# Performance work log

Measured on AMD Instinct MI355X. Metric: run time of the kernel, lower is better.

The kernel has to match this reference:

```python
import jax, jax.numpy as jnp
import numpy as np

N = 4096; E = 32768; H = 128; R = 32; L = 2
CUT_UP = 5.0; MAX_Z = 100

def cosine_cutoff(d):
    c = 0.5 * (jnp.cos(d * (np.pi / CUT_UP)) + 1.0)
    return c * (d < CUT_UP).astype(d.dtype)

def tensor_norm(t):
    return (t * t).sum((-2, -1))

def decompose_tensor(t):
    eye = jnp.eye(3, dtype=t.dtype)
    I = (jnp.trace(t, axis1=-2, axis2=-1) / 3.0)[..., None, None] * eye
    tT = jnp.swapaxes(t, -2, -1)
    A = 0.5 * (t - tT)
    S = 0.5 * (t + tT) - I
    return I, A, S

def vector_to_skewtensor(v):
    x, y, z = v[..., 0], v[..., 1], v[..., 2]
    o = jnp.zeros_like(x)
    return jnp.stack([o, -z, y, z, o, -x, -y, x, o], axis=-1).reshape(v.shape[:-1] + (3, 3))

def vector_to_symtensor(v):
    t = v[..., :, None] * v[..., None, :]
    eye = jnp.eye(3, dtype=v.dtype)
    I = (jnp.trace(t, axis1=-2, axis2=-1) / 3.0)[..., None, None] * eye
    return t - I  # symmetric already, 0.5*(t+t^T) == t

def cmix(T, W):  # nn.Linear(H,H,bias=False) over the channel dim of [N,H,3,3]
    return jnp.einsum('nhij,hk->nkij', T, W)

def layernorm(x, g, b, eps=1e-5):
    m = x.mean(-1, keepdims=True)
    v = ((x - m) ** 2).mean(-1, keepdims=True)
    return (x - m) / jnp.sqrt(v + eps) * g + b

def setup_inputs():
    key = jax.random.key(0)
    ks = iter(jax.random.split(key, 48))
    def nrm(shape, fan_in):
        return jax.random.normal(next(ks), shape, jnp.float32) / np.sqrt(fan_in)
    inp = {}
    inp['z'] = jax.random.randint(next(ks), (N,), 0, MAX_Z)
    inp['edge_index'] = jax.random.randint(next(ks), (2, E), 0, N)
    inp['edge_weight'] = jax.random.uniform(next(ks), (E,), jnp.float32) * CUT_UP
    inp['edge_vec'] = jax.random.normal(next(ks), (E, 3), jnp.float32)
    inp['edge_attr'] = jax.random.normal(next(ks), (E, R), jnp.float32)
    inp['emb_table'] = nrm((MAX_Z, H), H)
    inp['dp1_w'] = nrm((R, H), R); inp['dp1_b'] = jnp.zeros((H,))
    inp['dp2_w'] = nrm((R, H), R); inp['dp2_b'] = jnp.zeros((H,))
    inp['dp3_w'] = nrm((R, H), R); inp['dp3_b'] = jnp.zeros((H,))
    inp['emb2_w'] = nrm((2 * H, H), 2 * H); inp['emb2_b'] = jnp.zeros((H,))
    inp['tne_lt'] = nrm((3, H, H), H)
    inp['tne_s0_w'] = nrm((H, 2 * H), H); inp['tne_s0_b'] = jnp.zeros((2 * H,))
    inp['tne_s1_w'] = nrm((2 * H, 3 * H), 2 * H); inp['tne_s1_b'] = jnp.zeros((3 * H,))
    inp['ln_g'] = jnp.ones((H,)); inp['ln_b'] = jnp.zeros((H,))
    inp['msg_l0_w'] = nrm((L, R, H), R); inp['msg_l0_b'] = jnp.zeros((L, H))
    inp['msg_l1_w'] = nrm((L, H, 2 * H), H); inp['msg_l1_b'] = jnp.zeros((L, 2 * H))
    inp['msg_l2_w'] = nrm((L, 2 * H, 3 * H), 2 * H); inp['msg_l2_b'] = jnp.zeros((L, 3 * H))
    inp['msg_lx'] = nrm((L, 3, H, H), H)
    inp['msg_lt'] = nrm((L, 3, H, H), H)
    return inp

def _forward(z, edge_index, edge_weight, edge_vec, edge_attr, emb_table,
             dp1_w, dp1_b, dp2_w, dp2_b, dp3_w, dp3_b, emb2_w, emb2_b,
             tne_lt, tne_s0_w, tne_s0_b, tne_s1_w, tne_s1_b, ln_g, ln_b,
             msg_l0_w, msg_l0_b, msg_l1_w, msg_l1_b, msg_l2_w, msg_l2_b,
             msg_lx, msg_lt):
    src, dst = edge_index[0], edge_index[1]
    eye = jnp.eye(3, dtype=jnp.float32)
    segsum = lambda x: jax.ops.segment_sum(x, dst, num_segments=N)
    silu = jax.nn.silu
    # ---- TensorNeighborEmbedding ----
    Z = emb_table[z]                                     # [N,H]
    C = cosine_cutoff(edge_weight)                       # [E]
    W1 = (edge_attr @ dp1_w + dp1_b) * C[:, None]
    W2 = (edge_attr @ dp2_w + dp2_b) * C[:, None]
    W3 = (edge_attr @ dp3_w + dp3_b) * C[:, None]
    mask = (src != dst)[:, None]
    vn = jnp.linalg.norm(edge_vec, axis=-1, keepdims=True)
    ev = jnp.where(mask, edge_vec / jnp.maximum(vn, 1e-12), edge_vec)
    skew = vector_to_skewtensor(ev)                      # [E,3,3]
    sym = vector_to_symtensor(ev)                        # [E,3,3]
    Zij = jnp.concatenate([Z[dst], Z[src]], axis=-1) @ emb2_w + emb2_b  # [E,H]
    # I channel is a scaled identity per edge -> factor the eye out of the scatter
    In = segsum(Zij * W1)[..., None, None] * eye                         # [N,H,3,3]
    An = segsum((Zij * W2)[:, :, None, None] * skew[:, None])            # [N,H,3,3]
    Sn = segsum((Zij * W3)[:, :, None, None] * sym[:, None])             # [N,H,3,3]
    norm = layernorm(tensor_norm(In + An + Sn), ln_g, ln_b)              # [N,H]
    In = cmix(In, tne_lt[0]); An = cmix(An, tne_lt[1]); Sn = cmix(Sn, tne_lt[2])
    fsc = silu(silu(norm @ tne_s0_w + tne_s0_b) @ tne_s1_w + tne_s1_b).reshape(N, H, 3)
    X = (fsc[..., 0, None, None] * In + fsc[..., 1, None, None] * An
         + fsc[..., 2, None, None] * Sn)
    # ---- TensorMessage layers ----
    for l in range(L):
        ea = silu(edge_attr @ msg_l0_w[l] + msg_l0_b[l])
        ea = silu(ea @ msg_l1_w[l] + msg_l1_b[l])
        ea = silu(ea @ msg_l2_w[l] + msg_l2_b[l])
        ea = (ea * C[:, None]).reshape(E, H, 3)
        X = X / (tensor_norm(X) + 1.0)[..., None, None]
        I, A, S = decompose_tensor(X)
        I = cmix(I, msg_lx[l, 0]); A = cmix(A, msg_lx[l, 1]); S = cmix(S, msg_lx[l, 2])
        Y = I + A + S
        Im = segsum(ea[:, :, 0, None, None] * I[src])    # gather -> scale -> scatter
        Am = segsum(ea[:, :, 1, None, None] * A[src])
        Sm = segsum(ea[:, :, 2, None, None] * S[src])
        msg = Im + Am + Sm
        AB = msg @ Y + Y @ msg                           # batched 3x3 matmuls
        I, A, S = decompose_tensor(AB)
        d = (tensor_norm(I + A + S) + 1.0)[..., None, None]
        I = cmix(I / d, msg_lt[l, 0]); A = cmix(A / d, msg_lt[l, 1]); S = cmix(S / d, msg_lt[l, 2])
        dX = I + A + S
        dX = dX + dX @ dX
        X = X + dX
    return X

def reference(z, edge_index, edge_weight, edge_vec, edge_attr, emb_table,
              dp1_w, dp1_b, dp2_w, dp2_b, dp3_w, dp3_b, emb2_w, emb2_b,
              tne_lt, tne_s0_w, tne_s0_b, tne_s1_w, tne_s1_b, ln_g, ln_b,
              msg_l0_w, msg_l0_b, msg_l1_w, msg_l1_b, msg_l2_w, msg_l2_b,
              msg_lx, msg_lt):
    return _forward(z, edge_index, edge_weight, edge_vec, edge_attr, emb_table,
                    dp1_w, dp1_b, dp2_w, dp2_b, dp3_w, dp3_b, emb2_w, emb2_b,
                    tne_lt, tne_s0_w, tne_s0_b, tne_s1_w, tne_s1_b, ln_g, ln_b,
                    msg_l0_w, msg_l0_b, msg_l1_w, msg_l1_b, msg_l2_w, msg_l2_b,
                    msg_lx, msg_lt)
```

## Files before the change

kernel.cpp:

```cpp
#include <hip/hip_runtime.h>
#include <hip/hip_bf16.h>

typedef __hip_bfloat16 bf16;
typedef __attribute__((ext_vector_type(8))) short short8v;
typedef __attribute__((ext_vector_type(4))) float f32x4;

#define NN 4096
#define NE 32768
#define HH 128
#define MAXZ 100
#define TPB 8
#define NB 1


__device__ __forceinline__ float b2f(bf16 v){ return __bfloat162float(v); }
__device__ __forceinline__ float ldf(const float* p, size_t i){ return p[i]; }
__device__ __forceinline__ float ldf(const bf16*  p, size_t i){ return __bfloat162float(p[i]); }
__device__ __forceinline__ float siluf(float x){ return x * __builtin_amdgcn_rcpf(1.0f + __expf(-x)); }
__device__ __forceinline__ unsigned short f2bu(float x){
  bf16 h = __float2bfloat16(x);
  return *reinterpret_cast<unsigned short*>(&h);
}
__device__ __forceinline__ float bround(float x){
  bf16 h = __float2bfloat16(x);
// ... 17 lines not shown
__global__ void __launch_bounds__(256) k_count(const int* __restrict__ dst, int* __restrict__ counts){
  int e = blockIdx.x*256 + threadIdx.x;
  if (e < NE) atomicAdd(&counts[dst[e]], 1);
}

__global__ void __launch_bounds__(1024) k_scan(const int* __restrict__ counts, int* __restrict__ offsets, int* __restrict__ cursor){
  __shared__ int lds[1024];
  int t = threadIdx.x;
  int c0 = counts[4*t+0], c1 = counts[4*t+1], c2 = counts[4*t+2], c3 = counts[4*t+3];
  int s1 = c0+c1, s2 = s1+c2, s3 = s2+c3;
  lds[t] = s3;
  __syncthreads();
  for (int off=1; off<1024; off<<=1){
    int v = lds[t];
    int add = (t>=off)? lds[t-off] : 0;
    __syncthreads();
    lds[t] = v + add;
    __syncthreads();
  }
  int incl = lds[t];
  int base = incl - s3;
  offsets[4*t+0]=base;    offsets[4*t+1]=base+c0; offsets[4*t+2]=base+s1; offsets[4*t+3]=base+s2;
  cursor [4*t+0]=base;    cursor [4*t+1]=base+c0; cursor [4*t+2]=base+s1; cursor [4*t+3]=base+s2;
  if (t==1023) offsets[4096]=incl;
}

__global__ void __launch_bounds__(256) k_fill(const int* __restrict__ dst, const int* __restrict__ src,
                                              int* __restrict__ cursor,
                                              int* __restrict__ pos, int* __restrict__ csrc){
  int e = blockIdx.x*256 + threadIdx.x;
  if (e < NE){
    int p = atomicAdd(&cursor[dst[e]], 1);
    pos[e] = p;
    csrc[p] = src[e];
  }
}

template<typename T>
__device__ __forceinline__ void geom_impl(const T* ew, const T* evec,
    const int* src, const int* dst, const int* pos, float* gC, float* gVp){
  int e = blockIdx.x*256 + threadIdx.x;
  if (e >= NE) return;
  float d = ldf(ew, e);
  float c = 0.5f*(cosf(d*0.6283185307179586f)+1.0f);
  c = (d < 5.0f) ? c : 0.0f;
  gC[e] = c;
  float x = ldf(evec, (size_t)e*3+0), y = ldf(evec, (size_t)e*3+1), z = ldf(evec, (size_t)e*3+2);
  if (src[e] != dst[e]){
    float n = sqrtf(x*x+y*y+z*z);
    float inv = 1.0f/fmaxf(n, 1e-12f);
    x*=inv; y*=inv; z*=inv;
  }
  int p = pos[e];
  gVp[p*3+0]=x; gVp[p*3+1]=y; gVp[p*3+2]=z;
}
__global__ void __launch_bounds__(256) k_geom(const void* ew, const void* evec,
    const int* __restrict__ src, const int* __restrict__ dst, const int* __restrict__ pos,
    float* __restrict__ gC, float* __restrict__ gVp, const int* __restrict__ flag){
  if (flag[0]) geom_impl<float>((const float*)ew, (const float*)evec, src, dst, pos, gC, gVp);
  else         geom_impl<bf16 >((const bf16* )ew, (const bf16* )evec, src, dst, pos, gC, gVp);
}

template<typename T>
__device__ __forceinline__ void zemb_impl(const T* emb, const T* emb2_w,
    float* P1z, float* P2z, float* Zr){
  int zv = blockIdx.x, h = threadIdx.x;
  Zr[h] = ldf(emb, (size_t)zv*HH + h);
  __syncthreads();
  float p1=0.f, p2=0.f;
  for (int r=0;r<128;++r){
    float x = Zr[r];
    p1 += x*ldf(emb2_w, (size_t)r*HH+h);
    p2 += x*ldf(emb2_w, (size_t)(r+128)*HH+h);
  }
  P1z[zv*HH+h]=p1; P2z[zv*HH+h]=p2;
}
__global__ void __launch_bounds__(128) k_zemb(const void* emb, const void* emb2_w,
    float* __restrict__ P1z, float* __restrict__ P2z, const int* __restrict__ flag){
  __shared__ float Zr[128];
  if (flag[0]) zemb_impl<float>((const float*)emb, (const float*)emb2_w, P1z, P2z, Zr);
  else         zemb_impl<bf16 >((const bf16* )emb, (const bf16* )emb2_w, P1z, P2z, Zr);
}

__global__ void __launch_bounds__(256) k_cvt_attr(const void* in, unsigned short* __restrict__ out,
                                                  const int* __restrict__ flag){
  int i = blockIdx.x*256 + threadIdx.x;
  if (flag[0]) out[i] = f2bu(((const float*)in)[i]);
  else         out[i] = ((const unsigned short*)in)[i];
}

struct PackDescs {
  const void*     base[23];
  long            eoff[23];
  unsigned short* out[23];
  int K[23]; int N[23];
};
template<typename T>
__device__ __forceinline__ void pack_impl(const PackDescs& d){
  int y = blockIdx.y;
  int K = d.K[y], N = d.N[y];
  int ktiles = K>>5, ntiles = N>>4;
  int total = ktiles*ntiles*64;
  int idx = blockIdx.x*256 + threadIdx.x;
  if (idx >= total) return;
  int lane = idx & 63, tile = idx >> 6;
  int kt = tile % ktiles, nt = tile / ktiles;
  const T* W = (const T*)d.base[y] + d.eoff[y];
  int n = nt*16 + (lane&15), k0 = kt*32 + (lane>>4)*8;
  unsigned int t[8];
  #pragma unroll
  for (int j=0;j<8;++j) t[j] = f2bu(ldf(W, (size_t)(k0+j)*N + n));
  uint4 v;
  v.x = t[0] | (t[1]<<16);
  v.y = t[2] | (t[3]<<16);
  v.z = t[4] | (t[5]<<16);
  v.w = t[6] | (t[7]<<16);
  *reinterpret_cast<uint4*>(d.out[y] + ((size_t)tile*64 + lane)*8) = v;
}
__global__ void __launch_bounds__(256) k_pack(PackDescs d, const int* __restrict__ flag){
  if (flag[0]) pack_impl<float>(d);
  else         pack_impl<bf16 >(d);
}

template<typename T>
__device__ __forceinline__ void tne_edge_impl(
  const T* eattr, const int* src, const int* dst, const int* z, const int* pos,
  const T* dp1_w, const T* dp1_b, const T* dp2_w, const T* dp2_b,
  const T* dp3_w, const T* dp3_b, const T* emb2_b,
  const float* P1z, const float* P2z, const float* gC, bf16* eabuf,
  float (*attr)[32], int* zd, int* zs, int* ppos)
{
  int e0 = blockIdx.x*TPB;
  int h  = threadIdx.x;
  for (int i=h; i<TPB*32; i+=128) attr[i>>5][i&31] = ldf(eattr, (size_t)e0*32 + i);
  if (h < TPB){ int e=e0+h; zd[h]=z[dst[e]]; zs[h]=z[src[e]]; ppos[h]=pos[e]; }
  __syncthreads();
  float w1[TPB], w2[TPB], w3[TPB];
  float b1v=ldf(dp1_b,h), b2v=ldf(dp2_b,h), b3v=ldf(dp3_b,h);
  #pragma unroll
  for (int e=0;e<TPB;++e){ w1[e]=b1v; w2[e]=b2v; w3[e]=b3v; }
  for (int r=0;r<32;++r){
    float u1=ldf(dp1_w,(size_t)r*HH+h), u2=ldf(dp2_w,(size_t)r*HH+h), u3=ldf(dp3_w,(size_t)r*HH+h);
    #pragma unroll
    for (int e=0;e<TPB;++e){ float a=attr[e][r]; w1[e]+=a*u1; w2[e]+=a*u2; w3[e]+=a*u3; }
  }
  float eb = ldf(emb2_b,h);
  #pragma unroll
  for (int e=0;e<TPB;++e){
    float zij = P1z[zd[e]*HH+h] + P2z[zs[e]*HH+h] + eb;
    float c = gC[e0+e];
    bf16* p = eabuf + (size_t)ppos[e]*384;
    p[h]     = __float2bfloat16(zij*w1[e]*c);
    p[128+h] = __float2bfloat16(zij*w2[e]*c);
    p[256+h] = __float2bfloat16(zij*w3[e]*c);
  }
}
__global__ void __launch_bounds__(128) k_tne_edge(
  const void* eattr, const int* __restrict__ src, const int* __restrict__ dst,
  const int* __restrict__ z, const int* __restrict__ pos,
  const void* dp1_w, const void* dp1_b, const void* dp2_w, const void* dp2_b,
  const void* dp3_w, const void* dp3_b, const void* emb2_b,
  const float* __restrict__ P1z, const float* __restrict__ P2z,
  const float* __restrict__ gC, bf16* __restrict__ eabuf, const int* __restrict__ flag)
{
  __shared__ float attr[TPB][32];
  __shared__ int zd[TPB], zs[TPB], ppos[TPB];
  if (flag[0]) tne_edge_impl<float>((const float*)eattr, src, dst, z, pos,
      (const float*)dp1_w, (const float*)dp1_b, (const float*)dp2_w, (const float*)dp2_b,
      (const float*)dp3_w, (const float*)dp3_b, (const float*)emb2_b, P1z, P2z, gC, eabuf, attr, zd, zs, ppos);
  else tne_edge_impl<bf16>((const bf16*)eattr, src, dst, z, pos,
      (const bf16*)dp1_w, (const bf16*)dp1_b, (const bf16*)dp2_w, (const bf16*)dp2_b,
      (const bf16*)dp3_w, (const bf16*)dp3_b, (const bf16*)emb2_b, P1z, P2z, gC, eabuf, attr, zd, zs, ppos);
}

template<typename T>
__device__ __forceinline__ void tne_scat_impl(
  const int* offsets, const float* gVp, const bf16* eabuf,
  const T* ln_g, const T* ln_b, bf16* sm10, bf16* lnO, float* red)
{
  int n0 = blockIdx.x*NB, h = threadIdx.x;
  float tnv[NB];
  #pragma unroll
  for (int nn=0;nn<NB;++nn){
    int n = n0+nn;
    float a=0, v0=0,v1=0,v2=0, s0=0,s1=0,s2=0,s3=0,s4=0,s5=0;
    int beg = offsets[n], end = offsets[n+1];
    int i = beg;
    for (; i+4 <= end; i += 4){
      float c1[4],c2[4],c3[4],vx[4],vy[4],vz[4];
      #pragma unroll
      for (int u=0;u<4;++u){
        const bf16* p = eabuf + (size_t)(i+u)*384;
        c1[u]=b2f(p[h]); c2[u]=b2f(p[128+h]); c3[u]=b2f(p[256+h]);
        vx[u]=gVp[(i+u)*3+0]; vy[u]=gVp[(i+u)*3+1]; vz[u]=gVp[(i+u)*3+2];
      }
      #pragma unroll
      for (int u=0;u<4;++u){
        float tr3 = (vx[u]*vx[u]+vy[u]*vy[u]+vz[u]*vz[u])*(1.0f/3.0f);
        a  += c1[u];
        v0 += c2[u]*vx[u]; v1 += c2[u]*vy[u]; v2 += c2[u]*vz[u];
        s0 += c3[u]*(vx[u]*vx[u] - tr3); s1 += c3[u]*vx[u]*vy[u]; s2 += c3[u]*vx[u]*vz[u];
        s3 += c3[u]*(vy[u]*vy[u] - tr3); s4 += c3[u]*vy[u]*vz[u]; s5 += c3[u]*(vz[u]*vz[u] - tr3);
      }
    }
    for (; i<end; ++i){
      const bf16* p = eabuf + (size_t)i*384;
      float c1 = b2f(p[h]), c2 = b2f(p[128+h]), c3 = b2f(p[256+h]);
      float vx = gVp[i*3+0], vy = gVp[i*3+1], vz = gVp[i*3+2];
      float tr3 = (vx*vx+vy*vy+vz*vz)*(1.0f/3.0f);
      a  += c1;
      v0 += c2*vx; v1 += c2*vy; v2 += c2*vz;
      s0 += c3*(vx*vx - tr3); s1 += c3*vx*vy;          s2 += c3*vx*vz;
      s3 += c3*(vy*vy - tr3); s4 += c3*vy*vz;          s5 += c3*(vz*vz - tr3);
    }
    bf16* sp = sm10 + (size_t)n*1280;
    sp[0*128+h]=__float2bfloat16(a);
    sp[1*128+h]=__float2bfloat16(v0); sp[2*128+h]=__float2bfloat16(v1); sp[3*128+h]=__float2bfloat16(v2);
    sp[4*128+h]=__float2bfloat16(s0); sp[5*128+h]=__float2bfloat16(s1); sp[6*128+h]=__float2bfloat16(s2);
    sp[7*128+h]=__float2bfloat16(s3); sp[8*128+h]=__float2bfloat16(s4); sp[9*128+h]=__float2bfloat16(s5);
    tnv[nn] = 3.0f*a*a + 2.0f*(v0*v0+v1*v1+v2*v2)
            + s0*s0 + s3*s3 + s5*s5 + 2.0f*(s1*s1 + s2*s2 + s4*s4);
  }
  float gg = ldf(ln_g,h), bb = ldf(ln_b,h);
  #pragma unroll
  for (int nn=0;nn<NB;++nn){
    __syncthreads();
    red[h] = tnv[nn]; __syncthreads();
    for (int off=64; off>=1; off>>=1){ if (h<off) red[h]+=red[h+off]; __syncthreads(); }
    float mean = red[0]*(1.0f/128.0f);
    __syncthreads();
    float dm = tnv[nn] - mean;
    red[h] = dm*dm; __syncthreads();
    for (int off=64; off>=1; off>>=1){ if (h<off) red[h]+=red[h+off]; __syncthreads(); }
    float var = red[0]*(1.0f/128.0f);
    lnO[(size_t)(n0+nn)*128 + h] = __float2bfloat16(dm*rsqrtf(var+1e-5f)*gg + bb);
  }
}
__global__ void __launch_bounds__(128) k_tne_scat(
  const int* __restrict__ offsets, const float* __restrict__ gVp, const bf16* __restrict__ eabuf,
  const void* ln_g, const void* ln_b, bf16* __restrict__ sm10, bf16* __restrict__ lnO,
  const int* __restrict__ flag)
{
  __shared__ float red[128];
  if (flag[0]) tne_scat_impl<float>(offsets, gVp, eabuf, (const float*)ln_g, (const float*)ln_b, sm10, lnO, red);
  else         tne_scat_impl<bf16 >(offsets, gVp, eabuf, (const bf16* )ln_g, (const bf16* )ln_b, sm10, lnO, red);
}

template<typename T>
__device__ __forceinline__ void node_mlp_impl(
  const bf16* lnO, const unsigned short* ps0, const unsigned short* ps1,
  const T* b0, const T* b1, bf16* fsc3, unsigned short* h2p)
{
  int wid  = threadIdx.x >> 6;
  int lane = threadIdx.x & 63;
  int n0 = blockIdx.x*16;
  int m = lane & 15, g = lane >> 4;
  short8v aln[4];
  #pragma unroll
  for (int ks=0; ks<4; ++ks)
    aln[ks] = *reinterpret_cast<const short8v*>((const unsigned short*)lnO + (size_t)(n0+m)*128 + ks*32 + g*8);
  for (int nt=wid; nt<16; nt+=4){
    float bias = ldf(b0, nt*16+m);
    f32x4 acc = {bias,bias,bias,bias};
    #pragma unroll
    for (int ks=0; ks<4; ++ks){
      short8v b = *reinterpret_cast<const short8v*>(ps0 + ((size_t)(nt*4+ks)*64 + lane)*8);
      acc = __builtin_amdgcn_mfma_f32_16x16x32_bf16(aln[ks], b, acc, 0,0,0);
    }
    #pragma unroll
    for (int r=0;r<4;++r){
      int n = nt*16 + m, row = g*4 + r;
      h2p[(n>>5)*512 + (((n>>3)&3)*16+row)*8 + (n&7)] = f2bu(siluf(acc[r]));
    }
  }
  __syncthreads();
  short8v a3[8];
  #pragma unroll
  for (int ks=0; ks<8; ++ks) a3[ks] = *reinterpret_cast<const short8v*>(&h2p[ks*512 + lane*8]);
  for (int nt=wid; nt<24; nt+=4){
    float bias = ldf(b1, nt*16+m);
    f32x4 acc = {bias,bias,bias,bias};
    #pragma unroll
    for (int ks=0; ks<8; ++ks){
      short8v b = *reinterpret_cast<const short8v*>(ps1 + ((size_t)(nt*8+ks)*64 + lane)*8);
      acc = __builtin_amdgcn_mfma_f32_16x16x32_bf16(a3[ks], b, acc, 0,0,0);
    }
    #pragma unroll
    for (int r=0;r<4;++r){
      int n = nt*16 + m, row = g*4 + r;
      ((unsigned short*)fsc3)[(size_t)(n0+row)*384 + (n%3)*128 + (n/3)] = f2bu(siluf(acc[r]));
    }
  }
}
__global__ void __launch_bounds__(256) k_node_mlp(
  const bf16* __restrict__ lnO, const unsigned short* __restrict__ ps0,
  const unsigned short* __restrict__ ps1,
  const void* b0, const void* b1, bf16* __restrict__ fsc3, const int* __restrict__ flag)
{
  __shared__ __align__(16) unsigned short h2p[4096];
  if (flag[0]) node_mlp_impl<float>(lnO, ps0, ps1, (const float*)b0, (const float*)b1, fsc3, h2p);
  else         node_mlp_impl<bf16 >(lnO, ps0, ps1, (const bf16* )b0, (const bf16* )b1, fsc3, h2p);
}

__global__ void __launch_bounds__(256) k_tne_cmix(
  const bf16* __restrict__ sm10, const unsigned short* __restrict__ pwlt,
  const bf16* __restrict__ fsc3, float* __restrict__ X9)
{
  int wid  = threadIdx.x >> 6;
  int lane = threadIdx.x & 63;
  int n0 = blockIdx.x*16;
  int m = lane & 15, g = lane >> 4;
  f32x4 acc[10][2];
  #pragma unroll
  for (int c=0;c<10;++c){ acc[c][0]=(f32x4){0,0,0,0}; acc[c][1]=(f32x4){0,0,0,0}; }
  #pragma unroll
  for (int c=0;c<10;++c){
    int mat = (c==0) ? 0 : (c<4) ? 1 : 2;
    const unsigned short* bw = pwlt + (size_t)mat*16384;
    short8v af[4];
    #pragma unroll
    for (int ks=0; ks<4; ++ks)
      af[ks] = *reinterpret_cast<const short8v*>((const unsigned short*)sm10 + (size_t)(n0+m)*1280 + c*128 + ks*32 + g*8);
    #pragma unroll
    for (int t=0;t<2;++t){
      int nt = wid + t*4;
      #pragma unroll
      for (int ks=0; ks<4; ++ks){
        short8v b = *reinterpret_cast<const short8v*>(bw + ((size_t)(nt*4+ks)*64 + lane)*8);
        acc[c][t] = __builtin_amdgcn_mfma_f32_16x16x32_bf16(af[ks], b, acc[c][t], 0,0,0);
      }
    }
  }
  #pragma unroll
  for (int t=0;t<2;++t){
    int nt = wid + t*4;
    int h = nt*16 + m;
    #pragma unroll
    for (int r=0;r<4;++r){
      int node = n0 + g*4 + r;
      float am  = acc[0][t][r];
      float wm0 = acc[1][t][r], wm1 = acc[2][t][r], wm2 = acc[3][t][r];
      float t0 = acc[4][t][r], t1 = acc[5][t][r], t2 = acc[6][t][r];
      float t3 = acc[7][t][r], t4 = acc[8][t][r], t5 = acc[9][t][r];
      float f0 = b2f(fsc3[(size_t)node*384 + h]);
      float f1 = b2f(fsc3[(size_t)node*384 + 128 + h]);
      float f2 = b2f(fsc3[(size_t)node*384 + 256 + h]);
      float* xp = X9 + (size_t)node*1152;
      xp[0*128+h] = f0*am + f2*t0;
      xp[1*128+h] = -f1*wm2 + f2*t1;
      xp[2*128+h] =  f1*wm1 + f2*t2;
      xp[3*128+h] =  f1*wm2 + f2*t1;
      xp[4*128+h] = f0*am + f2*t3;
      xp[5*128+h] = -f1*wm0 + f2*t4;
      xp[6*128+h] = -f1*wm1 + f2*t2;
      xp[7*128+h] =  f1*wm0 + f2*t4;
      xp[8*128+h] = f0*am + f2*t5;
    }
  }
}

__global__ void __launch_bounds__(256) k_cmix_norm(
  float* __restrict__ X9, const unsigned short* __restrict__ pw, bf16* __restrict__ Y10)
{
  __shared__ __align__(16) unsigned short sst[16*1280];
  int n0 = blockIdx.x*16;
  int tid = threadIdx.x;
  #pragma unroll
  for (int it=0; it<8; ++it){
    int idx = it*256 + tid;
    int nn = idx >> 7, h = idx & 127;
    float* xp = X9 + (size_t)(n0+nn)*1152;
    float x00=xp[0*128+h], x01=xp[1*128+h], x02=xp[2*128+h];
    float x10=xp[3*128+h], x11=xp[4*128+h], x12=xp[5*128+h];
    float x20=xp[6*128+h], x21=xp[7*128+h], x22=xp[8*128+h];
    float tn = x00*x00+x01*x01+x02*x02+x10*x10+x11*x11+x12*x12+x20*x20+x21*x21+x22*x22;
    float inv = __builtin_amdgcn_rcpf(tn+1.0f);
    x00*=inv; x01*=inv; x02*=inv; x10*=inv; x11*=inv; x12*=inv; x20*=inv; x21*=inv; x22*=inv;
    xp[0*128+h]=x00; xp[1*128+h]=x01; xp[2*128+h]=x02;
    xp[3*128+h]=x10; xp[4*128+h]=x11; xp[5*128+h]=x12;
    xp[6*128+h]=x20; xp[7*128+h]=x21; xp[8*128+h]=x22;
    float a = (x00+x11+x22)*(1.0f/3.0f);
    unsigned short* sp = sst + (size_t)nn*1280;
    sp[0*128+h]=f2bu(a);
    sp[1*128+h]=f2bu(0.5f*(x21-x12));
    sp[2*128+h]=f2bu(0.5f*(x02-x20));
    sp[3*128+h]=f2bu(0.5f*(x10-x01));
    sp[4*128+h]=f2bu(x00-a);
    sp[5*128+h]=f2bu(0.5f*(x01+x10));
    sp[6*128+h]=f2bu(0.5f*(x02+x20));
    sp[7*128+h]=f2bu(x11-a);
    sp[8*128+h]=f2bu(0.5f*(x12+x21));
    sp[9*128+h]=f2bu(x22-a);
  }
  __syncthreads();
  int wid  = tid >> 6;
  int lane = tid & 63;
  int m = lane & 15, g = lane >> 4;
  f32x4 acc[10][2];
  #pragma unroll
  for (int c=0;c<10;++c){ acc[c][0]=(f32x4){0,0,0,0}; acc[c][1]=(f32x4){0,0,0,0}; }
  #pragma unroll
  for (int c=0;c<10;++c){
    int mat = (c==0) ? 0 : (c<4) ? 1 : 2;
    const unsigned short* bw = pw + (size_t)mat*16384;
    short8v af[4];
    #pragma unroll
    for (int ks=0; ks<4; ++ks)
      af[ks] = *reinterpret_cast<const short8v*>(&sst[(size_t)m*1280 + c*128 + ks*32 + g*8]);
    #pragma unroll
    for (int t=0;t<2;++t){
      int nt = wid + t*4;
      #pragma unroll
      for (int ks=0; ks<4; ++ks){
        short8v b = *reinterpret_cast<const short8v*>(bw + ((size_t)(nt*4+ks)*64 + lane)*8);
        acc[c][t] = __builtin_amdgcn_mfma_f32_16x16x32_bf16(af[ks], b, acc[c][t], 0,0,0);
      }
    }
  }
  #pragma unroll
  for (int t=0;t<2;++t){
    int nt = wid + t*4;
    int h = nt*16 + m;
    #pragma unroll
    for (int r=0;r<4;++r){
      int node = n0 + g*4 + r;
      unsigned short* op = (unsigned short*)Y10 + (size_t)node*1280;
      #pragma unroll
      for (int c=0;c<10;++c) op[c*128 + h] = f2bu(acc[c][t][r]);
    }
  }
}

template<typename T>
__device__ __forceinline__ void mfma_impl(
  const unsigned short* eattr_c, const float* gC, const int* pos,
  const unsigned short* p0, const unsigned short* p1, const unsigned short* p2,
  const T* b0, const T* b1, const T* b2,
  unsigned short* eabuf, unsigned short* buf, int* spos)
{
  int wid  = threadIdx.x >> 6;
  int lane = threadIdx.x & 63;
  int e0 = blockIdx.x*16;
  int m = lane & 15, g = lane >> 4;
  if (threadIdx.x < 16) spos[threadIdx.x] = pos[e0 + threadIdx.x];
  float cc[4];
  #pragma unroll
  for (int r=0;r<4;++r) cc[r] = gC[e0 + g*4 + r];
  unsigned short* h1p = buf;
  unsigned short* h2p = buf + 2048;
  short8v a1 = *reinterpret_cast<const short8v*>(eattr_c + (size_t)(e0+m)*32 + g*8);
  for (int nt=wid; nt<8; nt+=4){
    float bias = ldf(b0, nt*16+m);
    f32x4 acc = {bias,bias,bias,bias};
    short8v b = *reinterpret_cast<const short8v*>(p0 + ((size_t)nt*64 + lane)*8);
    acc = __builtin_amdgcn_mfma_f32_16x16x32_bf16(a1, b, acc, 0,0,0);
    #pragma unroll
    for (int r=0;r<4;++r){
      int n = nt*16 + m, row = g*4 + r;
      h1p[(n>>5)*512 + (((n>>3)&3)*16+row)*8 + (n&7)] = f2bu(siluf(acc[r]));
    }
  }
  __syncthreads();
  short8v a2[4];
  #pragma unroll
  for (int ks=0; ks<4; ++ks) a2[ks] = *reinterpret_cast<const short8v*>(&h1p[ks*512 + lane*8]);
  for (int nt=wid; nt<16; nt+=4){
    float bias = ldf(b1, nt*16+m);
    f32x4 acc = {bias,bias,bias,bias};
    #pragma unroll
    for (int ks=0; ks<4; ++ks){
      short8v b = *reinterpret_cast<const short8v*>(p1 + ((size_t)(nt*4+ks)*64 + lane)*8);
      acc = __builtin_amdgcn_mfma_f32_16x16x32_bf16(a2[ks], b, acc, 0,0,0);
    }
    #pragma unroll
    for (int r=0;r<4;++r){
      int n = nt*16 + m, row = g*4 + r;
      h2p[(n>>5)*512 + (((n>>3)&3)*16+row)*8 + (n&7)] = f2bu(siluf(acc[r]));
    }
  }
  __syncthreads();
  short8v a3[8];
  #pragma unroll
  for (int ks=0; ks<8; ++ks) a3[ks] = *reinterpret_cast<const short8v*>(&h2p[ks*512 + lane*8]);
  __syncthreads();
  for (int nt=wid; nt<24; nt+=4){
    float bias = ldf(b2, nt*16+m);
    f32x4 acc = {bias,bias,bias,bias};
    #pragma unroll
    for (int ks=0; ks<8; ++ks){
      short8v b = *reinterpret_cast<const short8v*>(p2 + ((size_t)(nt*8+ks)*64 + lane)*8);
      acc = __builtin_amdgcn_mfma_f32_16x16x32_bf16(a3[ks], b, acc, 0,0,0);
    }
    #pragma unroll
    for (int r=0;r<4;++r){
      int n = nt*16 + m, row = g*4 + r;
      float v = siluf(acc[r]) * cc[r];
      buf[row*408 + (n%3)*136 + (n/3)] = f2bu(v);
    }
  }
  __syncthreads();
  int r  = threadIdx.x >> 4;
  int ch = threadIdx.x & 15;
  size_t base = (size_t)spos[r]*384;
  #pragma unroll
  for (int seg=0; seg<3; ++seg){
    uint4 v = *reinterpret_cast<const uint4*>(&buf[r*408 + seg*136 + ch*8]);
    *reinterpret_cast<uint4*>(eabuf + base + (size_t)(seg*128 + ch*8)) = v;
  }
}
__global__ void __launch_bounds__(256) k_msg_edge_mfma(
  const unsigned short* __restrict__ eattr_c, const float* __restrict__ gC,
  const int* __restrict__ pos,
  const unsigned short* __restrict__ p0a, const unsigned short* __restrict__ p0b,
  const unsigned short* __restrict__ p1a, const unsigned short* __restrict__ p1b,
  const unsigned short* __restrict__ p2a, const unsigned short* __restrict__ p2b,
  const void* b0, const void* b1, const void* b2,
  unsigned short* __restrict__ eabuf_msg, const int* __restrict__ flag)
{
  __shared__ __align__(16) unsigned short buf[6528];
  __shared__ int spos[16];
  int l = blockIdx.y;
  const unsigned short* p0 = l ? p0b : p0a;
  const unsigned short* p1 = l ? p1b : p1a;
  const unsigned short* p2 = l ? p2b : p2a;
  unsigned short* eabuf = eabuf_msg + (size_t)l*NE*384;
  if (flag[0]) mfma_impl<float>(eattr_c, gC, pos, p0, p1, p2,
      (const float*)b0 + (long)l*128, (const float*)b1 + (long)l*256, (const float*)b2 + (long)l*384,
      eabuf, buf, spos);
  else mfma_impl<bf16>(eattr_c, gC, pos, p0, p1, p2,
      (const bf16*)b0 + (long)l*128, (const bf16*)b1 + (long)l*256, (const bf16*)b2 + (long)l*384,
      eabuf, buf, spos);
}

__global__ void __launch_bounds__(128) k_msg_sab(
  const int* __restrict__ offsets, const int* __restrict__ csrc,
  const bf16* __restrict__ eabuf, const bf16* __restrict__ Y10, bf16* __restrict__ smb)
{
  int n0 = blockIdx.x*NB, h = threadIdx.x;
  #pragma unroll
  for (int nn=0;nn<NB;++nn){
    int n = n0+nn;
    float am=0, vm0=0,vm1=0,vm2=0, smm0=0,smm1=0,smm2=0,smm3=0,smm4=0,smm5=0;
    int beg = offsets[n], end = offsets[n+1];
    int i = beg;
    for (; i+4 <= end; i += 4){
      int ss[4];
      #pragma unroll
      for (int u=0;u<4;++u){ ss[u] = csrc[i+u]; }
      float e0a[4], e1a[4], e2a[4];
      float y0[4],y1[4],y2[4],y3[4],y4[4],y5[4],y6[4],y7[4],y8[4],y9[4];
      #pragma unroll
      for (int u=0;u<4;++u){
        const bf16* ep = eabuf + (size_t)(i+u)*384;
        e0a[u]=b2f(ep[h]); e1a[u]=b2f(ep[128+h]); e2a[u]=b2f(ep[256+h]);
        const bf16* yp = Y10 + (size_t)ss[u]*1280;
        y0[u]=b2f(yp[0*128+h]); y1[u]=b2f(yp[1*128+h]); y2[u]=b2f(yp[2*128+h]);
        y3[u]=b2f(yp[3*128+h]); y4[u]=b2f(yp[4*128+h]); y5[u]=b2f(yp[5*128+h]);
        y6[u]=b2f(yp[6*128+h]); y7[u]=b2f(yp[7*128+h]); y8[u]=b2f(yp[8*128+h]);
        y9[u]=b2f(yp[9*128+h]);
      }
      #pragma unroll
      for (int u=0;u<4;++u){
        am   += e0a[u]*y0[u];
        vm0  += e1a[u]*y1[u]; vm1 += e1a[u]*y2[u]; vm2 += e1a[u]*y3[u];
        smm0 += e2a[u]*y4[u]; smm1 += e2a[u]*y5[u]; smm2 += e2a[u]*y6[u];
        smm3 += e2a[u]*y7[u]; smm4 += e2a[u]*y8[u]; smm5 += e2a[u]*y9[u];
      }
    }
    for (; i<end; ++i){
      int s = csrc[i];
      const bf16* ep = eabuf + (size_t)i*384;
      float e0 = b2f(ep[h]), e1 = b2f(ep[128+h]), e2 = b2f(ep[256+h]);
      const bf16* yp = Y10 + (size_t)s*1280;
      am   += e0*b2f(yp[0*128+h]);
      vm0  += e1*b2f(yp[1*128+h]); vm1 += e1*b2f(yp[2*128+h]); vm2 += e1*b2f(yp[3*128+h]);
      smm0 += e2*b2f(yp[4*128+h]); smm1 += e2*b2f(yp[5*128+h]); smm2 += e2*b2f(yp[6*128+h]);
      smm3 += e2*b2f(yp[7*128+h]); smm4 += e2*b2f(yp[8*128+h]); smm5 += e2*b2f(yp[9*128+h]);
    }
    const bf16* yp = Y10 + (size_t)n*1280;
    float aY=b2f(yp[0*128+h]), u0=b2f(yp[1*128+h]), u1=b2f(yp[2*128+h]), u2=b2f(yp[3*128+h]);
    float q0=b2f(yp[4*128+h]), q1=b2f(yp[5*128+h]), q2=b2f(yp[6*128+h]);
    float q3=b2f(yp[7*128+h]), q4=b2f(yp[8*128+h]), q5=b2f(yp[9*128+h]);
    float m00=am+smm0,   m01=-vm2+smm1, m02= vm1+smm2;
    float m10= vm2+smm1, m11=am+smm3,  m12=-vm0+smm4;
    float m20=-vm1+smm2, m21= vm0+smm4, m22=am+smm5;
    float y00=aY+q0,  y01=-u2+q1, y02= u1+q2;
    float y10= u2+q1, y11=aY+q3,  y12=-u0+q4;
    float y20=-u1+q2, y21= u0+q4, y22=aY+q5;
    float ab00 = m00*y00+m01*y10+m02*y20 + y00*m00+y01*m10+y02*m20;
    float ab01 = m00*y01+m01*y11+m02*y21 + y00*m01+y01*m11+y02*m21;
    float ab02 = m00*y02+m01*y12+m02*y22 + y00*m02+y01*m12+y02*m22;
    float ab10 = m10*y00+m11*y10+m12*y20 + y10*m00+y11*m10+y12*m20;
    float ab11 = m10*y01+m11*y11+m12*y21 + y10*m01+y11*m11+y12*m21;
    float ab12 = m10*y02+m11*y12+m12*y22 + y10*m02+y11*m12+y12*m22;
    float ab20 = m20*y00+m21*y10+m22*y20 + y20*m00+y21*m10+y22*m20;
    float ab21 = m20*y01+m21*y11+m22*y21 + y20*m01+y21*m11+y22*m21;
    float ab22 = m20*y02+m21*y12+m22*y22 + y20*m02+y21*m12+y22*m22;
    float a2 = (ab00+ab11+ab22)*(1.0f/3.0f);
    float w0 = 0.5f*(ab21-ab12), w1 = 0.5f*(ab02-ab20), w2 = 0.5f*(ab10-ab01);
    float t0 = ab00-a2, t1 = 0.5f*(ab01+ab10), t2 = 0.5f*(ab02+ab20);
    float t3 = ab11-a2, t4 = 0.5f*(ab12+ab21), t5 = ab22-a2;
    float dnm = ab00*ab00+ab01*ab01+ab02*ab02+ab10*ab10+ab11*ab11+ab12*ab12
              + ab20*ab20+ab21*ab21+ab22*ab22 + 1.0f;
    float inv = __builtin_amdgcn_rcpf(dnm);
    bf16* sp = smb + (size_t)n*1280;
    sp[0*128+h]=__float2bfloat16(a2*inv);
    sp[1*128+h]=__float2bfloat16(w0*inv); sp[2*128+h]=__float2bfloat16(w1*inv); sp[3*128+h]=__float2bfloat16(w2*inv);
    sp[4*128+h]=__float2bfloat16(t0*inv); sp[5*128+h]=__float2bfloat16(t1*inv); sp[6*128+h]=__float2bfloat16(t2*inv);
    sp[7*128+h]=__float2bfloat16(t3*inv); sp[8*128+h]=__float2bfloat16(t4*inv); sp[9*128+h]=__float2bfloat16(t5*inv);
  }
}

template<typename T>
__device__ __forceinline__ void cmix_fin_impl(
  const bf16* smb, const unsigned short* pw, float* X9, T* out, int write_out)
{
  int wid  = threadIdx.x >> 6;
  int lane = threadIdx.x & 63;
  int n0 = blockIdx.x*16;
  int m = lane & 15, g = lane >> 4;
  f32x4 acc[10][2];
  #pragma unroll
  for (int c=0;c<10;++c){ acc[c][0]=(f32x4){0,0,0,0}; acc[c][1]=(f32x4){0,0,0,0}; }
  #pragma unroll
  for (int c=0;c<10;++c){
    int mat = (c==0) ? 0 : (c<4) ? 1 : 2;
    const unsigned short* bw = pw + (size_t)mat*16384;
    short8v af[4];
    #pragma unroll
    for (int ks=0; ks<4; ++ks)
      af[ks] = *reinterpret_cast<const short8v*>((const unsigned short*)smb + (size_t)(n0+m)*1280 + c*128 + ks*32 + g*8);
    #pragma unroll
    for (int t=0;t<2;++t){
      int nt = wid + t*4;
      #pragma unroll
      for (int ks=0; ks<4; ++ks){
        short8v b = *reinterpret_cast<const short8v*>(bw + ((size_t)(nt*4+ks)*64 + lane)*8);
        acc[c][t] = __builtin_amdgcn_mfma_f32_16x16x32_bf16(af[ks], b, acc[c][t], 0,0,0);
      }
    }
  }
  #pragma unroll
  for (int t=0;t<2;++t){
    int nt = wid + t*4;
    int h = nt*16 + m;
    #pragma unroll
    for (int r=0;r<4;++r){
      int node = n0 + g*4 + r;
      float at  = bround(acc[0][t][r]);
      float vt0 = bround(acc[1][t][r]), vt1 = bround(acc[2][t][r]), vt2 = bround(acc[3][t][r]);
      float st0 = bround(acc[4][t][r]), st1 = bround(acc[5][t][r]), st2 = bround(acc[6][t][r]);
      float st3 = bround(acc[7][t][r]), st4 = bround(acc[8][t][r]), st5 = bround(acc[9][t][r]);
      float d00=at+st0,   d01=-vt2+st1, d02= vt1+st2;
      float d10= vt2+st1, d11=at+st3,  d12=-vt0+st4;
      float d20=-vt1+st2, d21= vt0+st4, d22=at+st5;
      float g00 = d00 + d00*d00+d01*d10+d02*d20;
      float g01 = d01 + d00*d01+d01*d11+d02*d21;
      float g02 = d02 + d00*d02+d01*d12+d02*d22;
      float g10 = d10 + d10*d00+d11*d10+d12*d20;
      float g11 = d11 + d10*d01+d11*d11+d12*d21;
      float g12 = d12 + d10*d02+d11*d12+d12*d22;
      float g20 = d20 + d20*d00+d21*d10+d22*d20;
      float g21 = d21 + d20*d01+d21*d11+d22*d21;
      float g22 = d22 + d20*d02+d21*d12+d22*d22;
      float* xp = X9 + (size_t)node*1152;
      float x00=xp[0*128+h]+g00, x01=xp[1*128+h]+g01, x02=xp[2*128+h]+g02;
      float x10=xp[3*128+h]+g10, x11=xp[4*128+h]+g11, x12=xp[5*128+h]+g12;
      float x20=xp[6*128+h]+g20, x21=xp[7*128+h]+g21, x22=xp[8*128+h]+g22;
      if (write_out){
        if (sizeof(T)==4){
          float* of = (float*)out + ((size_t)node*128 + h)*9;
          of[0]=x00; of[1]=x01; of[2]=x02; of[3]=x10; of[4]=x11; of[5]=x12; of[6]=x20; of[7]=x21; of[8]=x22;
        } else {
          bf16* ob = (bf16*)out + ((size_t)node*128 + h)*9;
          ob[0]=__float2bfloat16(x00); ob[1]=__float2bfloat16(x01); ob[2]=__float2bfloat16(x02);
          ob[3]=__float2bfloat16(x10); ob[4]=__float2bfloat16(x11); ob[5]=__float2bfloat16(x12);
          ob[6]=__float2bfloat16(x20); ob[7]=__float2bfloat16(x21); ob[8]=__float2bfloat16(x22);
        }
      } else {
        xp[0*128+h]=x00; xp[1*128+h]=x01; xp[2*128+h]=x02;
        xp[3*128+h]=x10; xp[4*128+h]=x11; xp[5*128+h]=x12;
        xp[6*128+h]=x20; xp[7*128+h]=x21; xp[8*128+h]=x22;
      }
    }
  }
}
__global__ void __launch_bounds__(256) k_cmix_fin(
  const bf16* __restrict__ smb, const unsigned short* __restrict__ pw,
  float* __restrict__ X9, void* __restrict__ out,
  const int* __restrict__ flag, int write_out)
{
  if (flag[0]) cmix_fin_impl<float>(smb, pw, X9, (float*)out, write_out);
  else         cmix_fin_impl<bf16 >(smb, pw, X9, (bf16* )out, write_out);
}

extern "C" void kernel_launch(void* const* d_in, const int* in_sizes, int n_in,
                              void* d_out, int out_size, void* d_ws, size_t ws_size,
                              hipStream_t stream)
{
  (void)in_sizes; (void)n_in; (void)out_size; (void)ws_size;
  const int* z    = (const int*)d_in[0];
  const int* eidx = (const int*)d_in[1];
  const int* src  = eidx;
  const int* dst  = eidx + NE;

  char* w = (char*)d_ws;
  int* flag    = (int*)w;   w += 64;
  int* counts  = (int*)w;   w += (size_t)NN*4;
  int* offsets = (int*)w;   w += (size_t)(NN+1)*4 + 60;
  int* cursor  = (int*)w;   w += (size_t)NN*4;
  int* pos     = (int*)w;   w += (size_t)NE*4;
  int* csrc    = (int*)w;   w += (size_t)NE*4;
  float* gC    = (float*)w; w += (size_t)NE*4;
  float* gVp   = (float*)w; w += (size_t)NE*12;
  float* P1z   = (float*)w; w += (size_t)MAXZ*HH*4;
  float* P2z   = (float*)w; w += (size_t)MAXZ*HH*4;
  bf16* eabuf  = (bf16*)w;  w += (size_t)NE*384*2;
  bf16* eabuf_msg = (bf16*)w; w += (size_t)2*NE*384*2;
  float* X9    = (float*)w; w += (size_t)NN*1152*4;
  bf16* Y10    = (bf16*)w;  w += (size_t)NN*1280*2;
  bf16* smb    = (bf16*)w;  w += (size_t)NN*1280*2;
  unsigned short* eattr_c = (unsigned short*)w; w += (size_t)NE*32*2;
  unsigned short* pw0[2]; unsigned short* pw1[2]; unsigned short* pw2[2];
  for (int l=0;l<2;++l){
    pw0[l] = (unsigned short*)w; w += 8*64*8*2;
    pw1[l] = (unsigned short*)w; w += 64*64*8*2;
    pw2[l] = (unsigned short*)w; w += 192*64*8*2;
  }
  unsigned short* pw_s0 = (unsigned short*)w; w += 64*64*8*2;
  unsigned short* pw_s1 = (unsigned short*)w; w += 192*64*8*2;
  unsigned short* pwlt  = (unsigned short*)w; w += 3*32*64*8*2;
  unsigned short* pwlx2 = (unsigned short*)w; w += 2*3*32*64*8*2;
  unsigned short* pwlt2 = (unsigned short*)w; w += 2*3*32*64*8*2;
  bf16* lnO    = (bf16*)w;  w += (size_t)NN*128*2;
  bf16* fsc3   = (bf16*)w;  w += (size_t)NN*384*2;
  bf16* sm10   = Y10;

  k_detect<<<1, 256, 0, stream>>>((const unsigned int*)d_in[4], flag);
  hipMemsetAsync(counts, 0, (size_t)NN*4, stream);
  k_count<<<NE/256, 256, 0, stream>>>(dst, counts);
  k_scan<<<1, 1024, 0, stream>>>(counts, offsets, cursor);
  k_fill<<<NE/256, 256, 0, stream>>>(dst, src, cursor, pos, csrc);
  k_geom<<<NE/256, 256, 0, stream>>>(d_in[2], d_in[3], src, dst, pos, gC, gVp, flag);
  k_zemb<<<MAXZ, 128, 0, stream>>>(d_in[5], d_in[12], P1z, P2z, flag);
  k_cvt_attr<<<NE*32/256, 256, 0, stream>>>(d_in[4], eattr_c, flag);

  PackDescs pd;
  for (int l=0;l<2;++l){
    pd.base[l*3+0] = d_in[21]; pd.eoff[l*3+0] = (long)l*32*128;
    pd.base[l*3+1] = d_in[23]; pd.eoff[l*3+1] = (long)l*128*256;
    pd.base[l*3+2] = d_in[25]; pd.eoff[l*3+2] = (long)l*256*384;
    pd.out[l*3+0] = pw0[l]; pd.K[l*3+0]=32;  pd.N[l*3+0]=128;
    pd.out[l*3+1] = pw1[l]; pd.K[l*3+1]=128; pd.N[l*3+1]=256;
    pd.out[l*3+2] = pw2[l]; pd.K[l*3+2]=256; pd.N[l*3+2]=384;
  }
  pd.base[6] = d_in[15]; pd.eoff[6] = 0; pd.out[6] = pw_s0; pd.K[6]=128; pd.N[6]=256;
  pd.base[7] = d_in[17]; pd.eoff[7] = 0; pd.out[7] = pw_s1; pd.K[7]=256; pd.N[7]=384;
  for (int c=0;c<3;++c){
    pd.base[8+c] = d_in[14]; pd.eoff[8+c] = (long)c*16384;
    pd.out[8+c] = pwlt + (size_t)c*16384; pd.K[8+c]=128; pd.N[8+c]=128;
  }
  for (int l=0;l<2;++l)
    for (int c=0;c<3;++c){
      pd.base[11+l*3+c] = d_in[27]; pd.eoff[11+l*3+c] = (long)(l*3+c)*16384;
      pd.out[11+l*3+c] = pwlx2 + (size_t)(l*3+c)*16384; pd.K[11+l*3+c]=128; pd.N[11+l*3+c]=128;
      pd.base[17+l*3+c] = d_in[28]; pd.eoff[17+l*3+c] = (long)(l*3+c)*16384;
      pd.out[17+l*3+c] = pwlt2 + (size_t)(l*3+c)*16384; pd.K[17+l*3+c]=128; pd.N[17+l*3+c]=128;
    }
  k_pack<<<dim3(48, 23), 256, 0, stream>>>(pd, flag);

  k_msg_edge_mfma<<<dim3(NE/16, 2), 256, 0, stream>>>(eattr_c, gC, pos,
      pw0[0], pw0[1], pw1[0], pw1[1], pw2[0], pw2[1],
      d_in[22], d_in[24], d_in[26],
      (unsigned short*)eabuf_msg, flag);

  k_tne_edge<<<NE/TPB, 128, 0, stream>>>(d_in[4], src, dst, z, pos,
      d_in[6], d_in[7], d_in[8], d_in[9], d_in[10], d_in[11], d_in[13],
      P1z, P2z, gC, eabuf, flag);
  k_tne_scat<<<NN/NB, 128, 0, stream>>>(offsets, gVp, eabuf,
      d_in[19], d_in[20], sm10, lnO, flag);
  k_node_mlp<<<NN/16, 256, 0, stream>>>(lnO, pw_s0, pw_s1, d_in[16], d_in[18], fsc3, flag);
  k_tne_cmix<<<NN/16, 256, 0, stream>>>(sm10, pwlt, fsc3, X9);

  for (int l=0; l<2; ++l){
    k_cmix_norm<<<NN/16, 256, 0, stream>>>(X9, pwlx2 + (size_t)l*3*16384, Y10);
    k_msg_sab<<<NN/NB, 128, 0, stream>>>(offsets, csrc,
        eabuf_msg + (size_t)l*NE*384, Y10, smb);
    k_cmix_fin<<<NN/16, 256, 0, stream>>>(smb, pwlt2 + (size_t)l*3*16384, X9, d_out,
        flag, (l==1)?1:0);
  }
}
```

Baseline: 224.9 us.

## Fuse tensor-norm and channel-mix into preceding cmix kernels across layers

Merges the embedding cmix with the first layer's normalize+cmix, and the layer-0 finalize with layer-1's normalize+cmix, so X9 is no longer written and then re-read between kernels. This drops two kernel launches and a full fp32 X9 round trip through global memory per fusion. In exchange each fused kernel holds two sets of MFMA accumulators and more shared-memory traffic, which raises register pressure and may lower occupancy.

```diff
diff --git a/kernel.cpp b/kernel.cpp
--- a/kernel.cpp
+++ b/kernel.cpp
@@ -343,25 +343,95 @@
   else         node_mlp_impl<bf16 >(lnO, ps0, ps1, (const bf16* )b0, (const bf16* )b1, fsc3, h2p);
 }
 
-__global__ void __launch_bounds__(256) k_tne_cmix(
+__global__ void __launch_bounds__(256) k_tne_cmix_norm(
   const bf16* __restrict__ sm10, const unsigned short* __restrict__ pwlt,
-  const bf16* __restrict__ fsc3, float* __restrict__ X9)
-{
+  const bf16* __restrict__ fsc3, const unsigned short* __restrict__ pwlx,
+  float* __restrict__ X9, bf16* __restrict__ Y10)
+{
+  __shared__ __align__(16) unsigned short sst[16*1280];
   int wid  = threadIdx.x >> 6;
   int lane = threadIdx.x & 63;
   int n0 = blockIdx.x*16;
   int m = lane & 15, g = lane >> 4;
+  {
+    f32x4 acc[10][2];
+    #pragma unroll
+    for (int c=0;c<10;++c){ acc[c][0]=(f32x4){0,0,0,0}; acc[c][1]=(f32x4){0,0,0,0}; }
+    #pragma unroll
+    for (int c=0;c<10;++c){
+      int mat = (c==0) ? 0 : (c<4) ? 1 : 2;
+      const unsigned short* bw = pwlt + (size_t)mat*16384;
+      short8v af[4];
+      #pragma unroll
+      for (int ks=0; ks<4; ++ks)
+        af[ks] = *reinterpret_cast<const short8v*>((const unsigned short*)sm10 + (size_t)(n0+m)*1280 + c*128 + ks*32 + g*8);
+      #pragma unroll
+      for (int t=0;t<2;++t){
+        int nt = wid + t*4;
+        #pragma unroll
+        for (int ks=0; ks<4; ++ks){
+          short8v b = *reinterpret_cast<const short8v*>(bw + ((size_t)(nt*4+ks)*64 + lane)*8);
+          acc[c][t] = __builtin_amdgcn_mfma_f32_16x16x32_bf16(af[ks], b, acc[c][t], 0,0,0);
+        }
+      }
+    }
+    #pragma unroll
+    for (int t=0;t<2;++t){
+      int nt = wid + t*4;
+      int h = nt*16 + m;
+      #pragma unroll
+      for (int r=0;r<4;++r){
+        int node = n0 + g*4 + r;
+        float am  = acc[0][t][r];
+        float wm0 = acc[1][t][r], wm1 = acc[2][t][r], wm2 = acc[3][t][r];
+        float t0 = acc[4][t][r], t1 = acc[5][t][r], t2 = acc[6][t][r];
+        float t3 = acc[7][t][r], t4 = acc[8][t][r], t5 = acc[9][t][r];
+        float f0 = b2f(fsc3[(size_t)node*384 + h]);
+        float f1 = b2f(fsc3[(size_t)node*384 + 128 + h]);
+        float f2 = b2f(fsc3[(size_t)node*384 + 256 + h]);
+        float x00 = f0*am + f2*t0;
+        float x01 = -f1*wm2 + f2*t1;
+        float x02 =  f1*wm1 + f2*t2;
+        float x10 =  f1*wm2 + f2*t1;
+        float x11 = f0*am + f2*t3;
+        float x12 = -f1*wm0 + f2*t4;
+        float x20 = -f1*wm1 + f2*t2;
+        float x21 =  f1*wm0 + f2*t4;
+        float x22 = f0*am + f2*t5;
+        float tn = x00*x00+x01*x01+x02*x02+x10*x10+x11*x11+x12*x12+x20*x20+x21*x21+x22*x22;
+        float inv = __builtin_amdgcn_rcpf(tn+1.0f);
+        x00*=inv; x01*=inv; x02*=inv; x10*=inv; x11*=inv; x12*=inv; x20*=inv; x21*=inv; x22*=inv;
+        float* xp = X9 + (size_t)node*1152;
+        xp[0*128+h]=x00; xp[1*128+h]=x01; xp[2*128+h]=x02;
+        xp[3*128+h]=x10; xp[4*128+h]=x11; xp[5*128+h]=x12;
+        xp[6*128+h]=x20; xp[7*128+h]=x21; xp[8*128+h]=x22;
+        float a = (x00+x11+x22)*(1.0f/3.0f);
+        unsigned short* sp = sst + (size_t)(g*4+r)*1280;
+        sp[0*128+h]=f2bu(a);
+        sp[1*128+h]=f2bu(0.5f*(x21-x12));
+        sp[2*128+h]=f2bu(0.5f*(x02-x20));
+        sp[3*128+h]=f2bu(0.5f*(x10-x01));
+        sp[4*128+h]=f2bu(x00-a);
+        sp[5*128+h]=f2bu(0.5f*(x01+x10));
+        sp[6*128+h]=f2bu(0.5f*(x02+x20));
+        sp[7*128+h]=f2bu(x11-a);
+        sp[8*128+h]=f2bu(0.5f*(x12+x21));
+        sp[9*128+h]=f2bu(x22-a);
+      }
+    }
+  }
+  __syncthreads();
   f32x4 acc[10][2];
   #pragma unroll
   for (int c=0;c<10;++c){ acc[c][0]=(f32x4){0,0,0,0}; acc[c][1]=(f32x4){0,0,0,0}; }
   #pragma unroll
   for (int c=0;c<10;++c){
     int mat = (c==0) ? 0 : (c<4) ? 1 : 2;
-    const unsigned short* bw = pwlt + (size_t)mat*16384;
+    const unsigned short* bw = pwlx + (size_t)mat*16384;
     short8v af[4];
     #pragma unroll
     for (int ks=0; ks<4; ++ks)
-      af[ks] = *reinterpret_cast<const short8v*>((const unsigned short*)sm10 + (size_t)(n0+m)*1280 + c*128 + ks*32 + g*8);
+      af[ks] = *reinterpret_cast<const short8v*>(&sst[(size_t)m*1280 + c*128 + ks*32 + g*8]);
     #pragma unroll
     for (int t=0;t<2;++t){
       int nt = wid + t*4;
@@ -379,71 +449,101 @@
     #pragma unroll
     for (int r=0;r<4;++r){
       int node = n0 + g*4 + r;
-      float am  = acc[0][t][r];
-      float wm0 = acc[1][t][r], wm1 = acc[2][t][r], wm2 = acc[3][t][r];
-      float t0 = acc[4][t][r], t1 = acc[5][t][r], t2 = acc[6][t][r];
-      float t3 = acc[7][t][r], t4 = acc[8][t][r], t5 = acc[9][t][r];
-      float f0 = b2f(fsc3[(size_t)node*384 + h]);
-      float f1 = b2f(fsc3[(size_t)node*384 + 128 + h]);
-      float f2 = b2f(fsc3[(size_t)node*384 + 256 + h]);
-      float* xp = X9 + (size_t)node*1152;
-      xp[0*128+h] = f0*am + f2*t0;
-      xp[1*128+h] = -f1*wm2 + f2*t1;
-      xp[2*128+h] =  f1*wm1 + f2*t2;
-      xp[3*128+h] =  f1*wm2 + f2*t1;
-      xp[4*128+h] = f0*am + f2*t3;
-      xp[5*128+h] = -f1*wm0 + f2*t4;
-      xp[6*128+h] = -f1*wm1 + f2*t2;
-      xp[7*128+h] =  f1*wm0 + f2*t4;
-      xp[8*128+h] = f0*am + f2*t5;
-    }
-  }
-}
-
-__global__ void __launch_bounds__(256) k_cmix_norm(
-  float* __restrict__ X9, const unsigned short* __restrict__ pw, bf16* __restrict__ Y10)
+      unsigned short* op = (unsigned short*)Y10 + (size_t)node*1280;
+      #pragma unroll
+      for (int c=0;c<10;++c) op[c*128 + h] = f2bu(acc[c][t][r]);
+    }
+  }
+}
+
+__global__ void __launch_bounds__(256) k_cmix_fin_norm(
+  const bf16* __restrict__ smb, const unsigned short* __restrict__ pwlt_l,
+  const unsigned short* __restrict__ pwlx_next,
+  float* __restrict__ X9, bf16* __restrict__ Y10)
 {
   __shared__ __align__(16) unsigned short sst[16*1280];
+  int wid  = threadIdx.x >> 6;
+  int lane = threadIdx.x & 63;
   int n0 = blockIdx.x*16;
-  int tid = threadIdx.x;
-  #pragma unroll
-  for (int it=0; it<8; ++it){
-    int idx = it*256 + tid;
-    int nn = idx >> 7, h = idx & 127;
-    float* xp = X9 + (size_t)(n0+nn)*1152;
-    float x00=xp[0*128+h], x01=xp[1*128+h], x02=xp[2*128+h];
-    float x10=xp[3*128+h], x11=xp[4*128+h], x12=xp[5*128+h];
-    float x20=xp[6*128+h], x21=xp[7*128+h], x22=xp[8*128+h];
-    float tn = x00*x00+x01*x01+x02*x02+x10*x10+x11*x11+x12*x12+x20*x20+x21*x21+x22*x22;
-    float inv = __builtin_amdgcn_rcpf(tn+1.0f);
-    x00*=inv; x01*=inv; x02*=inv; x10*=inv; x11*=inv; x12*=inv; x20*=inv; x21*=inv; x22*=inv;
-    xp[0*128+h]=x00; xp[1*128+h]=x01; xp[2*128+h]=x02;
-    xp[3*128+h]=x10; xp[4*128+h]=x11; xp[5*128+h]=x12;
-    xp[6*128+h]=x20; xp[7*128+h]=x21; xp[8*128+h]=x22;
-    float a = (x00+x11+x22)*(1.0f/3.0f);
-    unsigned short* sp = sst + (size_t)nn*1280;
-    sp[0*128+h]=f2bu(a);
-    sp[1*128+h]=f2bu(0.5f*(x21-x12));
-    sp[2*128+h]=f2bu(0.5f*(x02-x20));
-    sp[3*128+h]=f2bu(0.5f*(x10-x01));
-    sp[4*128+h]=f2bu(x00-a);
-    sp[5*128+h]=f2bu(0.5f*(x01+x10));
-    sp[6*128+h]=f2bu(0.5f*(x02+x20));
-    sp[7*128+h]=f2bu(x11-a);
-    sp[8*128+h]=f2bu(0.5f*(x12+x21));
-    sp[9*128+h]=f2bu(x22-a);
+  int m = lane & 15, g = lane >> 4;
+  {
+    f32x4 acc[10][2];
+    #pragma unroll
+    for (int c=0;c<10;++c){ acc[c][0]=(f32x4){0,0,0,0}; acc[c][1]=(f32x4){0,0,0,0}; }
+    #pragma unroll
+    for (int c=0;c<10;++c){
+      int mat = (c==0) ? 0 : (c<4) ? 1 : 2;
+      const unsigned short* bw = pwlt_l + (size_t)mat*16384;
+      short8v af[4];
+      #pragma unroll
+      for (int ks=0; ks<4; ++ks)
+        af[ks] = *reinterpret_cast<const short8v*>((const unsigned short*)smb + (size_t)(n0+m)*1280 + c*128 + ks*32 + g*8);
+      #pragma unroll
+      for (int t=0;t<2;++t){
+        int nt = wid + t*4;
+        #pragma unroll
+        for (int ks=0; ks<4; ++ks){
+          short8v b = *reinterpret_cast<const short8v*>(bw + ((size_t)(nt*4+ks)*64 + lane)*8);
+          acc[c][t] = __builtin_amdgcn_mfma_f32_16x16x32_bf16(af[ks], b, acc[c][t], 0,0,0);
+        }
+      }
+    }
+    #pragma unroll
+    for (int t=0;t<2;++t){
+      int nt = wid + t*4;
+      int h = nt*16 + m;
+      #pragma unroll
+      for (int r=0;r<4;++r){
+        int node = n0 + g*4 + r;
+        float at  = bround(acc[0][t][r]);
+        float vt0 = bround(acc[1][t][r]), vt1 = bround(acc[2][t][r]), vt2 = bround(acc[3][t][r]);
+        float st0 = bround(acc[4][t][r]), st1 = bround(acc[5][t][r]), st2 = bround(acc[6][t][r]);
+        float st3 = bround(acc[7][t][r]), st4 = bround(acc[8][t][r]), st5 = bround(acc[9][t][r]);
+        float d00=at+st0,   d01=-vt2+st1, d02= vt1+st2;
+        float d10= vt2+st1, d11=at+st3,  d12=-vt0+st4;
+        float d20=-vt1+st2, d21= vt0+st4, d22=at+st5;
+        float g00 = d00 + d00*d00+d01*d10+d02*d20;
+        float g01 = d01 + d00*d01+d01*d11+d02*d21;
+        float g02 = d02 + d00*d02+d01*d12+d02*d22;
+        float g10 = d10 + d10*d00+d11*d10+d12*d20;
+        float g11 = d11 + d10*d01+d11*d11+d12*d21;
+        float g12 = d12 + d10*d02+d11*d12+d12*d22;
+        float g20 = d20 + d20*d00+d21*d10+d22*d20;
+        float g21 = d21 + d20*d01+d21*d11+d22*d21;
+        float g22 = d22 + d20*d02+d21*d12+d22*d22;
+        float* xp = X9 + (size_t)node*1152;
+        float x00=xp[0*128+h]+g00, x01=xp[1*128+h]+g01, x02=xp[2*128+h]+g02;
+        float x10=xp[3*128+h]+g10, x11=xp[4*128+h]+g11, x12=xp[5*128+h]+g12;
+        float x20=xp[6*128+h]+g20, x21=xp[7*128+h]+g21, x22=xp[8*128+h]+g22;
+        float tn = x00*x00+x01*x01+x02*x02+x10*x10+x11*x11+x12*x12+x20*x20+x21*x21+x22*x22;
+        float inv = __builtin_amdgcn_rcpf(tn+1.0f);
+        x00*=inv; x01*=inv; x02*=inv; x10*=inv; x11*=inv; x12*=inv; x20*=inv; x21*=inv; x22*=inv;
+        xp[0*128+h]=x00; xp[1*128+h]=x01; xp[2*128+h]=x02;
+        xp[3*128+h]=x10; xp[4*128+h]=x11; xp[5*128+h]=x12;
+        xp[6*128+h]=x20; xp[7*128+h]=x21; xp[8*128+h]=x22;
+        float a = (x00+x11+x22)*(1.0f/3.0f);
+        unsigned short* sp = sst + (size_t)(g*4+r)*1280;
+        sp[0*128+h]=f2bu(a);
+        sp[1*128+h]=f2bu(0.5f*(x21-x12));
+        sp[2*128+h]=f2bu(0.5f*(x02-x20));
+        sp[3*128+h]=f2bu(0.5f*(x10-x01));
+        sp[4*128+h]=f2bu(x00-a);
+        sp[5*128+h]=f2bu(0.5f*(x01+x10));
+        sp[6*128+h]=f2bu(0.5f*(x02+x20));
+        sp[7*128+h]=f2bu(x11-a);
+        sp[8*128+h]=f2bu(0.5f*(x12+x21));
+        sp[9*128+h]=f2bu(x22-a);
+      }
+    }
   }
   __syncthreads();
-  int wid  = tid >> 6;
-  int lane = tid & 63;
-  int m = lane & 15, g = lane >> 4;
   f32x4 acc[10][2];
   #pragma unroll
   for (int c=0;c<10;++c){ acc[c][0]=(f32x4){0,0,0,0}; acc[c][1]=(f32x4){0,0,0,0}; }
   #pragma unroll
   for (int c=0;c<10;++c){
     int mat = (c==0) ? 0 : (c<4) ? 1 : 2;
-    const unsigned short* bw = pw + (size_t)mat*16384;
+    const unsigned short* bw = pwlx_next + (size_t)mat*16384;
     short8v af[4];
     #pragma unroll
     for (int ks=0; ks<4; ++ks)
@@ -821,13 +921,12 @@
   k_tne_scat<<<NN/NB, 128, 0, stream>>>(offsets, gVp, eabuf,
       d_in[19], d_in[20], sm10, lnO, flag);
   k_node_mlp<<<NN/16, 256, 0, stream>>>(lnO, pw_s0, pw_s1, d_in[16], d_in[18], fsc3, flag);
-  k_tne_cmix<<<NN/16, 256, 0, stream>>>(sm10, pwlt, fsc3, X9);
-
-  for (int l=0; l<2; ++l){
-    k_cmix_norm<<<NN/16, 256, 0, stream>>>(X9, pwlx2 + (size_t)l*3*16384, Y10);
-    k_msg_sab<<<NN/NB, 128, 0, stream>>>(offsets, csrc,
-        eabuf_msg + (size_t)l*NE*384, Y10, smb);
-    k_cmix_fin<<<NN/16, 256, 0, stream>>>(smb, pwlt2 + (size_t)l*3*16384, X9, d_out,
-        flag, (l==1)?1:0);
-  }
-}
+
+  k_tne_cmix_norm<<<NN/16, 256, 0, stream>>>(sm10, pwlt, fsc3, pwlx2, X9, Y10);
+
+  k_msg_sab<<<NN/NB, 128, 0, stream>>>(offsets, csrc, eabuf_msg, Y10, smb);
+  k_cmix_fin_norm<<<NN/16, 256, 0, stream>>>(smb, pwlt2, pwlx2 + (size_t)3*16384, X9, Y10);
+
+  k_msg_sab<<<NN/NB, 128, 0, stream>>>(offsets, csrc, eabuf_msg + (size_t)NE*384, Y10, smb);
+  k_cmix_fin<<<NN/16, 256, 0, stream>>>(smb, pwlt2 + (size_t)3*16384, X9, d_out, flag, 1);
+}
```

New measurement: 229.6 us. 2.1% more time.
